# Kernel tuning notes

Measured on AMD Instinct MI355X. Metric: run time of the kernel, lower is better.

Reference implementation:

```python
import jax, jax.numpy as jnp
import numpy as np

N_NODES = 100000
N_EDGES = 1600000
D = 128


def setup_inputs() -> dict:
    key = jax.random.key(0)
    k1, k2, k3 = jax.random.split(key, 3)
    x = jax.random.normal(k1, (N_NODES, D), dtype=jnp.float32)
    edge_index = jax.random.randint(k2, (2, N_EDGES), 0, N_NODES, dtype=jnp.int64)
    weight = jax.random.normal(k3, (D, D), dtype=jnp.float32) * (1.0 / np.sqrt(D))
    bias = jnp.zeros((D,), dtype=jnp.float32)
    return {"x": x, "edge_index": edge_index, "weight": weight, "bias": bias}


def reference(x, edge_index, weight, bias):
    # Eval-mode forward: dropout(p=0.5, training=False) is identity.
    N = x.shape[0]
    row, col = edge_index[0], edge_index[1]  # source -> target

    # gcn_norm: add self loops (weight 1), symmetric normalization
    loop = jnp.arange(N, dtype=edge_index.dtype)
    full_row = jnp.concatenate([row, loop])
    full_col = jnp.concatenate([col, loop])
    ew = jnp.ones(full_row.shape[0], dtype=x.dtype)
    deg = jax.ops.segment_sum(ew, full_col, num_segments=N)
    deg_inv_sqrt = jnp.where(deg > 0, jax.lax.rsqrt(jnp.maximum(deg, 1e-12)), 0.0)
    norm = deg_inv_sqrt[full_row] * ew * deg_inv_sqrt[full_col]  # [E+N]

    # linear transform then gather-scale-scatter aggregation
    h = x @ weight.T  # [N, D]
    msgs = h[full_row] * norm[:, None]  # [E+N, D]
    out = jax.ops.segment_sum(msgs, full_col, num_segments=N)
    out = out + bias
    return jax.nn.relu(out)
```

## Files before the change

### kernel.cpp

```cpp
#include <hip/hip_runtime.h>

#define N_NODES 100000
#define N_EDGES 1600000
#define D 128
#define N_STRIPS (N_NODES / 32)

#define BSH   9
#define NBKT  196
#define P_BLK 160
#define EPB   (N_EDGES / P_BLK)

typedef __bf16 bf16x4 __attribute__((ext_vector_type(4)));
typedef __bf16 bf16x8 __attribute__((ext_vector_type(8)));
typedef float  f32x4  __attribute__((ext_vector_type(4)));

__global__ __launch_bounds__(1024) void k_prep(const int* __restrict__ col,
                                               const float4* __restrict__ w4,
                                               int* __restrict__ bhist,
                                               bf16x4* __restrict__ wb4) {
    int tid = threadIdx.x, b = blockIdx.x;
    if (b == P_BLK) {
        for (int i = tid; i < (D * D) / 4; i += 1024) {
            float4 u = w4[i];
            bf16x4 p;
            p[0] = (__bf16)u.x; p[1] = (__bf16)u.y;
            p[2] = (__bf16)u.z; p[3] = (__bf16)u.w;
            wb4[i] = p;
        }
        return;
    }
    __shared__ int lh[NBKT];
    if (tid < NBKT) lh[tid] = 0;
    __syncthreads();
    int e0 = b * EPB;
    for (int e = e0 + tid; e < e0 + EPB; e += 1024)
        atomicAdd(&lh[col[e] >> BSH], 1);
    __syncthreads();
    if (tid < NBKT) bhist[tid * P_BLK + b] = lh[tid];
}

__global__ __launch_bounds__(256) void k_bscan(int* __restrict__ bhist,
                                               int* __restrict__ gtot) {
    __shared__ int buf[256];
    int k = blockIdx.x, t = threadIdx.x;
    int v = (t < P_BLK) ? bhist[k * P_BLK + t] : 0;
    buf[t] = v;
    __syncthreads();
    for (int off = 1; off < 256; off <<= 1) {
        int u = (t >= off) ? buf[t - off] : 0;
        __syncthreads();
        buf[t] += u;
        __syncthreads();
    }
    if (t < P_BLK) bhist[k * P_BLK + t] = buf[t] - v;
    if (t == 255) gtot[k] = buf[255];
}

__global__ __launch_bounds__(256) void k_gscan(const int* __restrict__ gtot,
                                               int* __restrict__ gstart) {
    __shared__ int buf[256];
    int t = threadIdx.x;
    int v = (t < NBKT) ? gtot[t] : 0;
    buf[t] = v;
    __syncthreads();
    for (int off = 1; off < 256; off <<= 1) {
        int u = (t >= off) ? buf[t - off] : 0;
        __syncthreads();
        buf[t] += u;
        __syncthreads();
    }
    if (t < NBKT) gstart[t] = buf[t] - v;
}

__global__ __launch_bounds__(1024) void k_cscatter(const int* __restrict__ row,
                                                   const int* __restrict__ col,
                                                   const int* __restrict__ bhist,
                                                   const int* __restrict__ gstart,
                                                   unsigned* __restrict__ grec) {
    __shared__ int cur[NBKT];
    int b = blockIdx.x, t = threadIdx.x;
    if (t < NBKT) cur[t] = gstart[t] + bhist[t * P_BLK + b];
    __syncthreads();
    int e0 = b * EPB;
    for (int e = e0 + t; e < e0 + EPB; e += 1024) {
        int c = col[e];
        unsigned rec = ((unsigned)row[e] << BSH) | (unsigned)(c & ((1 << BSH) - 1));
        int pos = atomicAdd(&cur[c >> BSH], 1);
        grec[pos] = rec;
    }
}

__global__ __launch_bounds__(1024) void k_fine(const unsigned* __restrict__ grec,
                                               const int* __restrict__ gtot,
                                               const int* __restrict__ gstart,
                                               int* __restrict__ deg,
                                               float* __restrict__ dis,
                                               int* __restrict__ start,
                                               int* __restrict__ srcs) {
    __shared__ int fh[512];
    __shared__ int fscan[512];
    int b = blockIdx.x;
    int tid = threadIdx.x;
    int cnt = gtot[b];
    int gs = gstart[b];
    if (tid < 512) fh[tid] = 0;
    __syncthreads();
    for (int i = tid; i < cnt; i += 1024)
        atomicAdd(&fh[grec[gs + i] & 511], 1);
    __syncthreads();
    int v = 0;
    if (tid < 512) { v = fh[tid]; fscan[tid] = v; }
    __syncthreads();
    for (int off = 1; off < 512; off <<= 1) {
        int u = 0;
        if (tid < 512 && tid >= off) u = fscan[tid - off];
        __syncthreads();
        if (tid < 512) fscan[tid] += u;
        __syncthreads();
    }
    if (tid < 512) {
        int excl = fscan[tid] - v;
        int node = (b << BSH) + tid;
        if (node < N_NODES) {
            deg[node] = v;
            dis[node] = rsqrtf((float)v + 1.0f);
            start[node] = gs + excl;
        }
        fh[tid] = excl;
    }
    __syncthreads();
    for (int i = tid; i < cnt; i += 1024) {
        unsigned r = grec[gs + i];
        int pos = atomicAdd(&fh[r & 511], 1);
        srcs[gs + pos] = (int)(r >> BSH);
    }
}

__global__ __launch_bounds__(256) void k_hx(const float* __restrict__ x,
                                            const __bf16* __restrict__ wb,
                                            const float* __restrict__ dis,
                                            __bf16* __restrict__ hb) {
    int wave = threadIdx.x >> 6;
    int lane = threadIdx.x & 63;
    int strip = blockIdx.x * 4 + wave;
    if (strip >= N_STRIPS) return;
    int m0 = strip * 32;
    int l15 = lane & 15;
    int kq  = lane >> 4;

    bf16x8 a[2][4];
    #pragma unroll
    for (int mt = 0; mt < 2; ++mt) {
        const float* ap = x + (size_t)(m0 + mt * 16 + l15) * D + kq * 8;
        #pragma unroll
        for (int ks = 0; ks < 4; ++ks) {
            float4 lo = *(const float4*)(ap + ks * 32);
            float4 hi = *(const float4*)(ap + ks * 32 + 4);
            bf16x8 t;
            t[0] = (__bf16)lo.x; t[1] = (__bf16)lo.y;
            t[2] = (__bf16)lo.z; t[3] = (__bf16)lo.w;
            t[4] = (__bf16)hi.x; t[5] = (__bf16)hi.y;
            t[6] = (__bf16)hi.z; t[7] = (__bf16)hi.w;
            a[mt][ks] = t;
        }
    }

    f32x4 acc[2][8] = {};
    #pragma unroll
    for (int ks = 0; ks < 4; ++ks) {
        #pragma unroll
        for (int nt = 0; nt < 8; ++nt) {
            bf16x8 b = *(const bf16x8*)(wb + (size_t)(nt * 16 + l15) * D + ks * 32 + kq * 8);
            acc[0][nt] = __builtin_amdgcn_mfma_f32_16x16x32_bf16(a[0][ks], b, acc[0][nt], 0, 0, 0);
            acc[1][nt] = __builtin_amdgcn_mfma_f32_16x16x32_bf16(a[1][ks], b, acc[1][nt], 0, 0, 0);
        }
    }

    float dsv[2][4];
    #pragma unroll
    for (int mt = 0; mt < 2; ++mt)
        #pragma unroll
        for (int r = 0; r < 4; ++r)
            dsv[mt][r] = dis[m0 + mt * 16 + kq * 4 + r];

    #pragma unroll
    for (int nt = 0; nt < 8; ++nt) {
        int colj = nt * 16 + l15;
        #pragma unroll
        for (int mt = 0; mt < 2; ++mt) {
            #pragma unroll
            for (int r = 0; r < 4; ++r) {
                int rowi = m0 + mt * 16 + kq * 4 + r;
                hb[(size_t)rowi * D + colj] = (__bf16)(acc[mt][nt][r] * dsv[mt][r]);
            }
        }
    }
}

__global__ __launch_bounds__(256) void k_aggregate(const int* __restrict__ srcs,
                                                   const int* __restrict__ start,
                                                   const int* __restrict__ deg,
                                                   const __bf16* __restrict__ hb,
                                                   const float* __restrict__ dis,
                                                   const float* __restrict__ bias,
                                                   float* __restrict__ out) {
    int node = (blockIdx.x * 256 + threadIdx.x) >> 6;
    int lane = threadIdx.x & 63;
    if (node >= N_NODES) return;
    int li   = lane & 31;
    int half = lane >> 5;
    int s = start[node];
    int n = deg[node];
    float dc = dis[node];
    const unsigned char* hbase = (const unsigned char*)hb;
    size_t boff = (size_t)li * 8;

    float acc0 = 0.f, acc1 = 0.f, acc2 = 0.f, acc3 = 0.f;

    for (int base = 0; base < n; base += 64) {
        int m = n - base; if (m > 64) m = 64;
        int src_l = (lane < m) ? srcs[s + base + lane] : 0;
        int i = 0;
        for (; i + 16 <= m; i += 16) {
            int sv[8]; uint2 av[8];
            #pragma unroll
            for (int j = 0; j < 8; ++j)
                sv[j] = __shfl(src_l, i + 2 * j + half);
            #pragma unroll
            for (int j = 0; j < 8; ++j)
                av[j] = *(const uint2*)(hbase + ((size_t)sv[j] * 256 + boff));
            #pragma unroll
            for (int j = 0; j < 8; ++j) {
                acc0 += __uint_as_float(av[j].x << 16);
                acc1 += __uint_as_float(av[j].x & 0xFFFF0000u);
                acc2 += __uint_as_float(av[j].y << 16);
                acc3 += __uint_as_float(av[j].y & 0xFFFF0000u);
            }
        }
        for (; i + 2 <= m; i += 2) {
            int sj = __shfl(src_l, i + half);
            uint2 a = *(const uint2*)(hbase + ((size_t)sj * 256 + boff));
            acc0 += __uint_as_float(a.x << 16);
            acc1 += __uint_as_float(a.x & 0xFFFF0000u);
            acc2 += __uint_as_float(a.y << 16);
            acc3 += __uint_as_float(a.y & 0xFFFF0000u);
        }
        if (i < m) {
            int sj = __shfl(src_l, i);
            if (half == 0) {
                uint2 a = *(const uint2*)(hbase + ((size_t)sj * 256 + boff));
                acc0 += __uint_as_float(a.x << 16);
                acc1 += __uint_as_float(a.x & 0xFFFF0000u);
                acc2 += __uint_as_float(a.y << 16);
                acc3 += __uint_as_float(a.y & 0xFFFF0000u);
            }
        }
    }

    acc0 += __shfl_xor(acc0, 32);
    acc1 += __shfl_xor(acc1, 32);
    acc2 += __shfl_xor(acc2, 32);
    acc3 += __shfl_xor(acc3, 32);

    if (half == 0) {
        uint2 a = *(const uint2*)(hbase + ((size_t)node * 256 + boff));
        acc0 += __uint_as_float(a.x << 16);
        acc1 += __uint_as_float(a.x & 0xFFFF0000u);
        acc2 += __uint_as_float(a.y << 16);
        acc3 += __uint_as_float(a.y & 0xFFFF0000u);

        float4 b4 = *(const float4*)(bias + li * 4);
        float4 r;
        r.x = fmaxf(acc0 * dc + b4.x, 0.f);
        r.y = fmaxf(acc1 * dc + b4.y, 0.f);
        r.z = fmaxf(acc2 * dc + b4.z, 0.f);
        r.w = fmaxf(acc3 * dc + b4.w, 0.f);
        *(float4*)(out + (size_t)node * D + li * 4) = r;
    }
}

extern "C" void kernel_launch(void* const* d_in, const int* in_sizes, int n_in,
                              void* d_out, int out_size, void* d_ws, size_t ws_size,
                              hipStream_t stream) {
    const float* x    = (const float*)d_in[0];
    const int*   ei   = (const int*)d_in[1];
    const float* w    = (const float*)d_in[2];
    const float* bias = (const float*)d_in[3];
    float* out = (float*)d_out;

    char* ws = (char*)d_ws;
    int*      deg    = (int*)ws;              ws += N_NODES * 4;
    float*    dis    = (float*)ws;            ws += N_NODES * 4;
    int*      start  = (int*)ws;              ws += N_NODES * 4;
    int*      bhist  = (int*)ws;              ws += NBKT * P_BLK * 4;
    int*      gtot   = (int*)ws;              ws += 256 * 4;
    int*      gstart = (int*)ws;              ws += 256 * 4;
    __bf16*   wb     = (__bf16*)ws;           ws += D * D * 2;
    unsigned* grec   = (unsigned*)ws;         ws += (size_t)N_EDGES * 4;
    int*      srcs   = (int*)ws;              ws += (size_t)N_EDGES * 4;
    __bf16*   hb     = (__bf16*)ws;

    const int* row = ei;
    const int* col = ei + N_EDGES;

    k_prep     <<<P_BLK + 1, 1024, 0, stream>>>(col, (const float4*)w, bhist, (bf16x4*)wb);
    k_bscan    <<<NBKT, 256, 0, stream>>>(bhist, gtot);
    k_gscan    <<<1, 256, 0, stream>>>(gtot, gstart);
    k_cscatter <<<P_BLK, 1024, 0, stream>>>(row, col, bhist, gstart, grec);
    k_fine     <<<NBKT, 1024, 0, stream>>>(grec, gtot, gstart, deg, dis, start, srcs);
    k_hx       <<<(N_STRIPS + 3) / 4, 256, 0, stream>>>(x, wb, dis, hb);
    k_aggregate<<<(N_NODES * 64 + 255) / 256, 256, 0, stream>>>(srcs, start, deg, hb, dis, bias, out);
}
```

Measured before the change: 227.8 us.

## Replace two-level bucket sort CSR build with global atomic counting sort

```diff
diff --git a/kernel.cpp b/kernel.cpp
--- a/kernel.cpp
+++ b/kernel.cpp
@@ -5,22 +5,21 @@
 #define D 128
 #define N_STRIPS (N_NODES / 32)
 
-#define BSH   9
-#define NBKT  196
-#define P_BLK 160
-#define EPB   (N_EDGES / P_BLK)
+#define E4      (N_EDGES / 4)
+#define HB_BLK  391
+#define NSCB    98
 
 typedef __bf16 bf16x4 __attribute__((ext_vector_type(4)));
 typedef __bf16 bf16x8 __attribute__((ext_vector_type(8)));
 typedef float  f32x4  __attribute__((ext_vector_type(4)));
 
-__global__ __launch_bounds__(1024) void k_prep(const int* __restrict__ col,
+__global__ __launch_bounds__(1024) void k_hist(const int4* __restrict__ col4,
                                                const float4* __restrict__ w4,
-                                               int* __restrict__ bhist,
+                                               int* __restrict__ deg,
                                                bf16x4* __restrict__ wb4) {
-    int tid = threadIdx.x, b = blockIdx.x;
-    if (b == P_BLK) {
-        for (int i = tid; i < (D * D) / 4; i += 1024) {
+    int b = blockIdx.x, t = threadIdx.x;
+    if (b == HB_BLK) {
+        for (int i = t; i < (D * D) / 4; i += 1024) {
             float4 u = w4[i];
             bf16x4 p;
             p[0] = (__bf16)u.x; p[1] = (__bf16)u.y;
@@ -29,111 +28,74 @@
         }
         return;
     }
-    __shared__ int lh[NBKT];
-    if (tid < NBKT) lh[tid] = 0;
-    __syncthreads();
-    int e0 = b * EPB;
-    for (int e = e0 + tid; e < e0 + EPB; e += 1024)
-        atomicAdd(&lh[col[e] >> BSH], 1);
-    __syncthreads();
-    if (tid < NBKT) bhist[tid * P_BLK + b] = lh[tid];
-}
-
-__global__ __launch_bounds__(256) void k_bscan(int* __restrict__ bhist,
-                                               int* __restrict__ gtot) {
-    __shared__ int buf[256];
-    int k = blockIdx.x, t = threadIdx.x;
-    int v = (t < P_BLK) ? bhist[k * P_BLK + t] : 0;
+    int i = b * 1024 + t;
+    if (i < E4) {
+        int4 c = col4[i];
+        atomicAdd(&deg[c.x], 1);
+        atomicAdd(&deg[c.y], 1);
+        atomicAdd(&deg[c.z], 1);
+        atomicAdd(&deg[c.w], 1);
+    }
+}
+
+__global__ __launch_bounds__(1024) void k_scanl(const int* __restrict__ deg,
+                                                int* __restrict__ start,
+                                                int* __restrict__ btot) {
+    __shared__ int buf[1024];
+    int b = blockIdx.x, t = threadIdx.x;
+    int i = b * 1024 + t;
+    int v = (i < N_NODES) ? deg[i] : 0;
     buf[t] = v;
     __syncthreads();
-    for (int off = 1; off < 256; off <<= 1) {
+    for (int off = 1; off < 1024; off <<= 1) {
         int u = (t >= off) ? buf[t - off] : 0;
         __syncthreads();
         buf[t] += u;
         __syncthreads();
     }
-    if (t < P_BLK) bhist[k * P_BLK + t] = buf[t] - v;
-    if (t == 255) gtot[k] = buf[255];
-}
-
-__global__ __launch_bounds__(256) void k_gscan(const int* __restrict__ gtot,
-                                               int* __restrict__ gstart) {
-    __shared__ int buf[256];
-    int t = threadIdx.x;
-    int v = (t < NBKT) ? gtot[t] : 0;
-    buf[t] = v;
+    if (i < N_NODES) start[i] = buf[t] - v;
+    if (t == 1023) btot[b] = buf[1023];
+}
+
+__global__ __launch_bounds__(1024) void k_fixup(const int* __restrict__ deg,
+                                                const int* __restrict__ btot,
+                                                int* __restrict__ start,
+                                                int* __restrict__ cur,
+                                                float* __restrict__ dis) {
+    __shared__ int red[128];
+    int b = blockIdx.x, t = threadIdx.x;
+    if (t < 128) red[t] = (t < b) ? btot[t] : 0;
     __syncthreads();
-    for (int off = 1; off < 256; off <<= 1) {
-        int u = (t >= off) ? buf[t - off] : 0;
+    for (int off = 64; off > 0; off >>= 1) {
+        if (t < off) red[t] += red[t + off];
         __syncthreads();
-        buf[t] += u;
-        __syncthreads();
-    }
-    if (t < NBKT) gstart[t] = buf[t] - v;
-}
-
-__global__ __launch_bounds__(1024) void k_cscatter(const int* __restrict__ row,
-                                                   const int* __restrict__ col,
-                                                   const int* __restrict__ bhist,
-                                                   const int* __restrict__ gstart,
-                                                   unsigned* __restrict__ grec) {
-    __shared__ int cur[NBKT];
-    int b = blockIdx.x, t = threadIdx.x;
-    if (t < NBKT) cur[t] = gstart[t] + bhist[t * P_BLK + b];
-    __syncthreads();
-    int e0 = b * EPB;
-    for (int e = e0 + t; e < e0 + EPB; e += 1024) {
-        int c = col[e];
-        unsigned rec = ((unsigned)row[e] << BSH) | (unsigned)(c & ((1 << BSH) - 1));
-        int pos = atomicAdd(&cur[c >> BSH], 1);
-        grec[pos] = rec;
-    }
-}
-
-__global__ __launch_bounds__(1024) void k_fine(const unsigned* __restrict__ grec,
-                                               const int* __restrict__ gtot,
-                                               const int* __restrict__ gstart,
-                                               int* __restrict__ deg,
-                                               float* __restrict__ dis,
-                                               int* __restrict__ start,
-                                               int* __restrict__ srcs) {
-    __shared__ int fh[512];
-    __shared__ int fscan[512];
-    int b = blockIdx.x;
-    int tid = threadIdx.x;
-    int cnt = gtot[b];
-    int gs = gstart[b];
-    if (tid < 512) fh[tid] = 0;
-    __syncthreads();
-    for (int i = tid; i < cnt; i += 1024)
-        atomicAdd(&fh[grec[gs + i] & 511], 1);
-    __syncthreads();
-    int v = 0;
-    if (tid < 512) { v = fh[tid]; fscan[tid] = v; }
-    __syncthreads();
-    for (int off = 1; off < 512; off <<= 1) {
-        int u = 0;
-        if (tid < 512 && tid >= off) u = fscan[tid - off];
-        __syncthreads();
-        if (tid < 512) fscan[tid] += u;
-        __syncthreads();
-    }
-    if (tid < 512) {
-        int excl = fscan[tid] - v;
-        int node = (b << BSH) + tid;
-        if (node < N_NODES) {
-            deg[node] = v;
-            dis[node] = rsqrtf((float)v + 1.0f);
-            start[node] = gs + excl;
-        }
-        fh[tid] = excl;
-    }
-    __syncthreads();
-    for (int i = tid; i < cnt; i += 1024) {
-        unsigned r = grec[gs + i];
-        int pos = atomicAdd(&fh[r & 511], 1);
-        srcs[gs + pos] = (int)(r >> BSH);
-    }
+    }
+    int boff = red[0];
+    int i = b * 1024 + t;
+    if (i < N_NODES) {
+        int s = start[i] + boff;
+        start[i] = s;
+        cur[i]   = s;
+        dis[i]   = rsqrtf((float)deg[i] + 1.0f);
+    }
+}
+
+__global__ __launch_bounds__(1024) void k_scatter(const int4* __restrict__ row4,
+                                                  const int4* __restrict__ col4,
+                                                  int* __restrict__ cur,
+                                                  int* __restrict__ srcs) {
+    int i = blockIdx.x * 1024 + threadIdx.x;
+    if (i >= E4) return;
+    int4 r = row4[i];
+    int4 c = col4[i];
+    int p0 = atomicAdd(&cur[c.x], 1);
+    int p1 = atomicAdd(&cur[c.y], 1);
+    int p2 = atomicAdd(&cur[c.z], 1);
+    int p3 = atomicAdd(&cur[c.w], 1);
+    srcs[p0] = r.x << 8;
+    srcs[p1] = r.y << 8;
+    srcs[p2] = r.z << 8;
+    srcs[p3] = r.w << 8;
 }
 
 __global__ __launch_bounds__(256) void k_hx(const float* __restrict__ x,
@@ -228,7 +190,7 @@
                 sv[j] = __shfl(src_l, i + 2 * j + half);
             #pragma unroll
             for (int j = 0; j < 8; ++j)
-                av[j] = *(const uint2*)(hbase + ((size_t)sv[j] * 256 + boff));
+                av[j] = *(const uint2*)(hbase + ((size_t)sv[j] + boff));
             #pragma unroll
             for (int j = 0; j < 8; ++j) {
                 acc0 += __uint_as_float(av[j].x << 16);
@@ -239,7 +201,7 @@
         }
         for (; i + 2 <= m; i += 2) {
             int sj = __shfl(src_l, i + half);
-            uint2 a = *(const uint2*)(hbase + ((size_t)sj * 256 + boff));
+            uint2 a = *(const uint2*)(hbase + ((size_t)sj + boff));
             acc0 += __uint_as_float(a.x << 16);
             acc1 += __uint_as_float(a.x & 0xFFFF0000u);
             acc2 += __uint_as_float(a.y << 16);
@@ -248,7 +210,7 @@
         if (i < m) {
             int sj = __shfl(src_l, i);
             if (half == 0) {
-                uint2 a = *(const uint2*)(hbase + ((size_t)sj * 256 + boff));
+                uint2 a = *(const uint2*)(hbase + ((size_t)sj + boff));
                 acc0 += __uint_as_float(a.x << 16);
                 acc1 += __uint_as_float(a.x & 0xFFFF0000u);
                 acc2 += __uint_as_float(a.y << 16);
@@ -292,22 +254,20 @@
     int*      deg    = (int*)ws;              ws += N_NODES * 4;
     float*    dis    = (float*)ws;            ws += N_NODES * 4;
     int*      start  = (int*)ws;              ws += N_NODES * 4;
-    int*      bhist  = (int*)ws;              ws += NBKT * P_BLK * 4;
-    int*      gtot   = (int*)ws;              ws += 256 * 4;
-    int*      gstart = (int*)ws;              ws += 256 * 4;
+    int*      cur    = (int*)ws;              ws += N_NODES * 4;
+    int*      btot   = (int*)ws;              ws += 256 * 4;
     __bf16*   wb     = (__bf16*)ws;           ws += D * D * 2;
-    unsigned* grec   = (unsigned*)ws;         ws += (size_t)N_EDGES * 4;
     int*      srcs   = (int*)ws;              ws += (size_t)N_EDGES * 4;
     __bf16*   hb     = (__bf16*)ws;
 
     const int* row = ei;
     const int* col = ei + N_EDGES;
 
-    k_prep     <<<P_BLK + 1, 1024, 0, stream>>>(col, (const float4*)w, bhist, (bf16x4*)wb);
-    k_bscan    <<<NBKT, 256, 0, stream>>>(bhist, gtot);
-    k_gscan    <<<1, 256, 0, stream>>>(gtot, gstart);
-    k_cscatter <<<P_BLK, 1024, 0, stream>>>(row, col, bhist, gstart, grec);
-    k_fine     <<<NBKT, 1024, 0, stream>>>(grec, gtot, gstart, deg, dis, start, srcs);
-    k_hx       <<<(N_STRIPS + 3) / 4, 256, 0, stream>>>(x, wb, dis, hb);
+    hipMemsetAsync(deg, 0, N_NODES * 4, stream);
+    k_hist   <<<HB_BLK + 1, 1024, 0, stream>>>((const int4*)col, (const float4*)w, deg, (bf16x4*)wb);
+    k_scanl  <<<NSCB, 1024, 0, stream>>>(deg, start, btot);
+    k_fixup  <<<NSCB, 1024, 0, stream>>>(deg, btot, start, cur, dis);
+    k_scatter<<<HB_BLK, 1024, 0, stream>>>((const int4*)row, (const int4*)col, cur, srcs);
+    k_hx     <<<(N_STRIPS + 3) / 4, 256, 0, stream>>>(x, wb, dis, hb);
     k_aggregate<<<(N_NODES * 64 + 255) / 256, 256, 0, stream>>>(srcs, start, deg, hb, dis, bias, out);
 }
```

After: 369.3 us. +62.1%, slower.

## Fuse CSR-build kernels into one cooperative kernel with grid syncs and LDS edge caching

Applied to the files above, without the earlier changes.

```diff
diff --git a/kernel.cpp b/kernel.cpp
--- a/kernel.cpp
+++ b/kernel.cpp
@@ -1,4 +1,7 @@
 #include <hip/hip_runtime.h>
+#include <hip/hip_cooperative_groups.h>
+
+namespace cg = cooperative_groups;
 
 #define N_NODES 100000
 #define N_EDGES 1600000
@@ -7,19 +10,58 @@
 
 #define BSH   9
 #define NBKT  196
-#define P_BLK 160
-#define EPB   (N_EDGES / P_BLK)
+#define GRID_P 256
+#define EPB2  (N_EDGES / GRID_P)
 
 typedef __bf16 bf16x4 __attribute__((ext_vector_type(4)));
 typedef __bf16 bf16x8 __attribute__((ext_vector_type(8)));
 typedef float  f32x4  __attribute__((ext_vector_type(4)));
 
-__global__ __launch_bounds__(1024) void k_prep(const int* __restrict__ col,
+__global__ __launch_bounds__(1024) void k_part(const int* __restrict__ row,
+                                               const int* __restrict__ col,
                                                const float4* __restrict__ w4,
                                                int* __restrict__ bhist,
+                                               int* __restrict__ gtot,
+                                               int* __restrict__ gstart,
+                                               unsigned* __restrict__ grec,
+                                               int* __restrict__ srcs,
+                                               int* __restrict__ deg,
+                                               float* __restrict__ dis,
+                                               int* __restrict__ start,
                                                bf16x4* __restrict__ wb4) {
-    int tid = threadIdx.x, b = blockIdx.x;
-    if (b == P_BLK) {
+    cg::grid_group grid = cg::this_grid();
+    __shared__ int smem[13312];
+    int b = blockIdx.x, tid = threadIdx.x;
+    int* rowc = smem;
+    int* colc = smem + 6250;
+    int* aux  = smem + 12500;
+
+    if (tid < 256) aux[tid] = 0;
+    __syncthreads();
+    int e0 = b * EPB2;
+    for (int i = tid; i < EPB2; i += 1024) {
+        int r = row[e0 + i], c = col[e0 + i];
+        rowc[i] = r; colc[i] = c;
+        atomicAdd(&aux[c >> BSH], 1);
+    }
+    __syncthreads();
+    if (tid < NBKT) bhist[tid * GRID_P + b] = aux[tid];
+    grid.sync();
+
+    if (b < NBKT) {
+        int v = 0;
+        if (tid < 256) { v = bhist[b * GRID_P + tid]; aux[tid] = v; }
+        __syncthreads();
+        for (int off = 1; off < 256; off <<= 1) {
+            int u = 0;
+            if (tid < 256 && tid >= off) u = aux[tid - off];
+            __syncthreads();
+            if (tid < 256) aux[tid] += u;
+            __syncthreads();
+        }
+        if (tid < 256) bhist[b * GRID_P + tid] = aux[tid] - v;
+        if (tid == 255) gtot[b] = aux[255];
+    } else if (b == NBKT) {
         for (int i = tid; i < (D * D) / 4; i += 1024) {
             float4 u = w4[i];
             bf16x4 p;
@@ -27,112 +69,72 @@
             p[2] = (__bf16)u.z; p[3] = (__bf16)u.w;
             wb4[i] = p;
         }
-        return;
-    }
-    __shared__ int lh[NBKT];
-    if (tid < NBKT) lh[tid] = 0;
+    }
+    grid.sync();
+
+    if (b == 0) {
+        int v = 0;
+        if (tid < 256) { v = (tid < NBKT) ? gtot[tid] : 0; aux[tid] = v; }
+        __syncthreads();
+        for (int off = 1; off < 256; off <<= 1) {
+            int u = 0;
+            if (tid < 256 && tid >= off) u = aux[tid - off];
+            __syncthreads();
+            if (tid < 256) aux[tid] += u;
+            __syncthreads();
+        }
+        if (tid < NBKT) gstart[tid] = aux[tid] - v;
+    }
+    grid.sync();
+
+    if (tid < NBKT) aux[tid] = gstart[tid] + bhist[tid * GRID_P + b];
     __syncthreads();
-    int e0 = b * EPB;
-    for (int e = e0 + tid; e < e0 + EPB; e += 1024)
-        atomicAdd(&lh[col[e] >> BSH], 1);
-    __syncthreads();
-    if (tid < NBKT) bhist[tid * P_BLK + b] = lh[tid];
-}
-
-__global__ __launch_bounds__(256) void k_bscan(int* __restrict__ bhist,
-                                               int* __restrict__ gtot) {
-    __shared__ int buf[256];
-    int k = blockIdx.x, t = threadIdx.x;
-    int v = (t < P_BLK) ? bhist[k * P_BLK + t] : 0;
-    buf[t] = v;
-    __syncthreads();
-    for (int off = 1; off < 256; off <<= 1) {
-        int u = (t >= off) ? buf[t - off] : 0;
-        __syncthreads();
-        buf[t] += u;
-        __syncthreads();
-    }
-    if (t < P_BLK) bhist[k * P_BLK + t] = buf[t] - v;
-    if (t == 255) gtot[k] = buf[255];
-}
-
-__global__ __launch_bounds__(256) void k_gscan(const int* __restrict__ gtot,
-                                               int* __restrict__ gstart) {
-    __shared__ int buf[256];
-    int t = threadIdx.x;
-    int v = (t < NBKT) ? gtot[t] : 0;
-    buf[t] = v;
-    __syncthreads();
-    for (int off = 1; off < 256; off <<= 1) {
-        int u = (t >= off) ? buf[t - off] : 0;
-        __syncthreads();
-        buf[t] += u;
-        __syncthreads();
-    }
-    if (t < NBKT) gstart[t] = buf[t] - v;
-}
-
-__global__ __launch_bounds__(1024) void k_cscatter(const int* __restrict__ row,
-                                                   const int* __restrict__ col,
-                                                   const int* __restrict__ bhist,
-                                                   const int* __restrict__ gstart,
-                                                   unsigned* __restrict__ grec) {
-    __shared__ int cur[NBKT];
-    int b = blockIdx.x, t = threadIdx.x;
-    if (t < NBKT) cur[t] = gstart[t] + bhist[t * P_BLK + b];
-    __syncthreads();
-    int e0 = b * EPB;
-    for (int e = e0 + t; e < e0 + EPB; e += 1024) {
-        int c = col[e];
-        unsigned rec = ((unsigned)row[e] << BSH) | (unsigned)(c & ((1 << BSH) - 1));
-        int pos = atomicAdd(&cur[c >> BSH], 1);
-        grec[pos] = rec;
-    }
-}
-
-__global__ __launch_bounds__(1024) void k_fine(const unsigned* __restrict__ grec,
-                                               const int* __restrict__ gtot,
-                                               const int* __restrict__ gstart,
-                                               int* __restrict__ deg,
-                                               float* __restrict__ dis,
-                                               int* __restrict__ start,
-                                               int* __restrict__ srcs) {
-    __shared__ int fh[512];
-    __shared__ int fscan[512];
-    int b = blockIdx.x;
-    int tid = threadIdx.x;
-    int cnt = gtot[b];
-    int gs = gstart[b];
-    if (tid < 512) fh[tid] = 0;
-    __syncthreads();
-    for (int i = tid; i < cnt; i += 1024)
-        atomicAdd(&fh[grec[gs + i] & 511], 1);
-    __syncthreads();
-    int v = 0;
-    if (tid < 512) { v = fh[tid]; fscan[tid] = v; }
-    __syncthreads();
-    for (int off = 1; off < 512; off <<= 1) {
-        int u = 0;
-        if (tid < 512 && tid >= off) u = fscan[tid - off];
-        __syncthreads();
-        if (tid < 512) fscan[tid] += u;
-        __syncthreads();
-    }
-    if (tid < 512) {
-        int excl = fscan[tid] - v;
-        int node = (b << BSH) + tid;
-        if (node < N_NODES) {
-            deg[node] = v;
-            dis[node] = rsqrtf((float)v + 1.0f);
-            start[node] = gs + excl;
-        }
-        fh[tid] = excl;
-    }
-    __syncthreads();
-    for (int i = tid; i < cnt; i += 1024) {
-        unsigned r = grec[gs + i];
-        int pos = atomicAdd(&fh[r & 511], 1);
-        srcs[gs + pos] = (int)(r >> BSH);
+    for (int i = tid; i < EPB2; i += 1024) {
+        int c = colc[i];
+        int pos = atomicAdd(&aux[c >> BSH], 1);
+        grec[pos] = ((unsigned)rowc[i] << BSH) | (unsigned)(c & ((1 << BSH) - 1));
+    }
+    grid.sync();
+
+    if (b < NBKT) {
+        int cnt = gtot[b], gs = gstart[b];
+        int* cache = smem;
+        int* fh    = smem + 12288;
+        int* fsc   = smem + 12800;
+        if (tid < 512) fh[tid] = 0;
+        __syncthreads();
+        for (int i = tid; i < cnt; i += 1024) {
+            unsigned r = grec[gs + i];
+            if (i < 12288) cache[i] = (int)r;
+            atomicAdd(&fh[r & 511], 1);
+        }
+        __syncthreads();
+        int v = 0;
+        if (tid < 512) { v = fh[tid]; fsc[tid] = v; }
+        __syncthreads();
+        for (int off = 1; off < 512; off <<= 1) {
+            int u = 0;
+            if (tid < 512 && tid >= off) u = fsc[tid - off];
+            __syncthreads();
+            if (tid < 512) fsc[tid] += u;
+            __syncthreads();
+        }
+        if (tid < 512) {
+            int excl = fsc[tid] - v;
+            int node = (b << BSH) + tid;
+            if (node < N_NODES) {
+                deg[node]   = v;
+                dis[node]   = rsqrtf((float)v + 1.0f);
+                start[node] = gs + excl;
+            }
+            fh[tid] = excl;
+        }
+        __syncthreads();
+        for (int i = tid; i < cnt; i += 1024) {
+            unsigned r = (i < 12288) ? (unsigned)cache[i] : grec[gs + i];
+            int pos = atomicAdd(&fh[r & 511], 1);
+            srcs[gs + pos] = (int)((r >> BSH) << 8);
+        }
     }
 }
 
@@ -228,7 +230,7 @@
                 sv[j] = __shfl(src_l, i + 2 * j + half);
             #pragma unroll
             for (int j = 0; j < 8; ++j)
-                av[j] = *(const uint2*)(hbase + ((size_t)sv[j] * 256 + boff));
+                av[j] = *(const uint2*)(hbase + ((size_t)sv[j] + boff));
             #pragma unroll
             for (int j = 0; j < 8; ++j) {
                 acc0 += __uint_as_float(av[j].x << 16);
@@ -239,7 +241,7 @@
         }
         for (; i + 2 <= m; i += 2) {
             int sj = __shfl(src_l, i + half);
-            uint2 a = *(const uint2*)(hbase + ((size_t)sj * 256 + boff));
+            uint2 a = *(const uint2*)(hbase + ((size_t)sj + boff));
             acc0 += __uint_as_float(a.x << 16);
             acc1 += __uint_as_float(a.x & 0xFFFF0000u);
             acc2 += __uint_as_float(a.y << 16);
@@ -248,7 +250,7 @@
         if (i < m) {
             int sj = __shfl(src_l, i);
             if (half == 0) {
-                uint2 a = *(const uint2*)(hbase + ((size_t)sj * 256 + boff));
+                uint2 a = *(const uint2*)(hbase + ((size_t)sj + boff));
                 acc0 += __uint_as_float(a.x << 16);
                 acc1 += __uint_as_float(a.x & 0xFFFF0000u);
                 acc2 += __uint_as_float(a.y << 16);
@@ -292,7 +294,7 @@
     int*      deg    = (int*)ws;              ws += N_NODES * 4;
     float*    dis    = (float*)ws;            ws += N_NODES * 4;
     int*      start  = (int*)ws;              ws += N_NODES * 4;
-    int*      bhist  = (int*)ws;              ws += NBKT * P_BLK * 4;
+    int*      bhist  = (int*)ws;              ws += NBKT * GRID_P * 4;
     int*      gtot   = (int*)ws;              ws += 256 * 4;
     int*      gstart = (int*)ws;              ws += 256 * 4;
     __bf16*   wb     = (__bf16*)ws;           ws += D * D * 2;
@@ -302,12 +304,14 @@
 
     const int* row = ei;
     const int* col = ei + N_EDGES;
-
-    k_prep     <<<P_BLK + 1, 1024, 0, stream>>>(col, (const float4*)w, bhist, (bf16x4*)wb);
-    k_bscan    <<<NBKT, 256, 0, stream>>>(bhist, gtot);
-    k_gscan    <<<1, 256, 0, stream>>>(gtot, gstart);
-    k_cscatter <<<P_BLK, 1024, 0, stream>>>(row, col, bhist, gstart, grec);
-    k_fine     <<<NBKT, 1024, 0, stream>>>(grec, gtot, gstart, deg, dis, start, srcs);
+    const float4* w4 = (const float4*)w;
+    bf16x4* wb4 = (bf16x4*)wb;
+
+    void* kargs[] = {(void*)&row, (void*)&col, (void*)&w4, (void*)&bhist,
+                     (void*)&gtot, (void*)&gstart, (void*)&grec, (void*)&srcs,
+                     (void*)&deg, (void*)&dis, (void*)&start, (void*)&wb4};
+    hipLaunchCooperativeKernel((const void*)k_part, dim3(GRID_P), dim3(1024),
+                               kargs, 0, stream);
     k_hx       <<<(N_STRIPS + 3) / 4, 256, 0, stream>>>(x, wb, dis, hb);
     k_aggregate<<<(N_NODES * 64 + 255) / 256, 256, 0, stream>>>(srcs, start, deg, hb, dis, bias, out);
 }
```

Result: slower. 349.4 us (+53.4%).

## Fuse fine CSR scatter into aggregation via per-block shared-memory source lists

Applied to the files above, without the earlier changes.

```diff
diff --git a/kernel.cpp b/kernel.cpp
--- a/kernel.cpp
+++ b/kernel.cpp
@@ -9,6 +9,7 @@
 #define NBKT  196
 #define P_BLK 160
 #define EPB   (N_EDGES / P_BLK)
+#define SL_CAP 6144
 
 typedef __bf16 bf16x4 __attribute__((ext_vector_type(4)));
 typedef __bf16 bf16x8 __attribute__((ext_vector_type(8)));
@@ -90,15 +91,14 @@
     }
 }
 
-__global__ __launch_bounds__(1024) void k_fine(const unsigned* __restrict__ grec,
-                                               const int* __restrict__ gtot,
-                                               const int* __restrict__ gstart,
-                                               int* __restrict__ deg,
-                                               float* __restrict__ dis,
-                                               int* __restrict__ start,
-                                               int* __restrict__ srcs) {
+__global__ __launch_bounds__(1024) void k_fine2(const unsigned* __restrict__ grec,
+                                                const int* __restrict__ gtot,
+                                                const int* __restrict__ gstart,
+                                                int* __restrict__ deg,
+                                                float* __restrict__ dis,
+                                                int* __restrict__ start) {
     __shared__ int fh[512];
-    __shared__ int fscan[512];
+    __shared__ int fsc[512];
     int b = blockIdx.x;
     int tid = threadIdx.x;
     int cnt = gtot[b];
@@ -109,30 +109,22 @@
         atomicAdd(&fh[grec[gs + i] & 511], 1);
     __syncthreads();
     int v = 0;
-    if (tid < 512) { v = fh[tid]; fscan[tid] = v; }
+    if (tid < 512) { v = fh[tid]; fsc[tid] = v; }
     __syncthreads();
     for (int off = 1; off < 512; off <<= 1) {
         int u = 0;
-        if (tid < 512 && tid >= off) u = fscan[tid - off];
-        __syncthreads();
-        if (tid < 512) fscan[tid] += u;
+        if (tid < 512 && tid >= off) u = fsc[tid - off];
+        __syncthreads();
+        if (tid < 512) fsc[tid] += u;
         __syncthreads();
     }
     if (tid < 512) {
-        int excl = fscan[tid] - v;
         int node = (b << BSH) + tid;
         if (node < N_NODES) {
-            deg[node] = v;
-            dis[node] = rsqrtf((float)v + 1.0f);
-            start[node] = gs + excl;
-        }
-        fh[tid] = excl;
-    }
-    __syncthreads();
-    for (int i = tid; i < cnt; i += 1024) {
-        unsigned r = grec[gs + i];
-        int pos = atomicAdd(&fh[r & 511], 1);
-        srcs[gs + pos] = (int)(r >> BSH);
+            deg[node]   = v;
+            dis[node]   = rsqrtf((float)v + 1.0f);
+            start[node] = gs + fsc[tid] - v;
+        }
     }
 }
 
@@ -197,85 +189,124 @@
     }
 }
 
-__global__ __launch_bounds__(256) void k_aggregate(const int* __restrict__ srcs,
+__global__ __launch_bounds__(512) void k_aggregate(const unsigned* __restrict__ grec,
+                                                   const int* __restrict__ gtot,
+                                                   const int* __restrict__ gstart,
                                                    const int* __restrict__ start,
                                                    const int* __restrict__ deg,
                                                    const __bf16* __restrict__ hb,
                                                    const float* __restrict__ dis,
                                                    const float* __restrict__ bias,
                                                    float* __restrict__ out) {
-    int node = (blockIdx.x * 256 + threadIdx.x) >> 6;
-    int lane = threadIdx.x & 63;
-    if (node >= N_NODES) return;
+    __shared__ int srcsL[SL_CAP];
+    __shared__ int cur[128];
+    __shared__ int sbase_s;
+    int blk = blockIdx.x;
+    int b  = blk >> 2;
+    int sl = blk & 3;
+    int cnt = gtot[b];
+    int gs  = gstart[b];
+    int node0 = (b << BSH) + sl * 128;
+    int t = threadIdx.x;
+
+    if (t == 0)
+        sbase_s = (node0 < N_NODES) ? start[node0] : gs + cnt;
+    if (t < 128) {
+        int nd = node0 + t;
+        cur[t] = (nd < N_NODES) ? start[nd] : gs + cnt;
+    }
+    __syncthreads();
+    int sbase = sbase_s;
+    if (t < 128) cur[t] -= sbase;
+    __syncthreads();
+
+    int lo = sl * 128;
+    for (int i = t; i < cnt; i += 512) {
+        unsigned r = grec[gs + i];
+        int s = (int)(r & 511) - lo;
+        if ((unsigned)s < 128u) {
+            int p = atomicAdd(&cur[s], 1);
+            if (p < SL_CAP) srcsL[p] = (int)((r >> BSH) << 8);
+        }
+    }
+    __syncthreads();
+
+    int wave = t >> 6;
+    int lane = t & 63;
     int li   = lane & 31;
     int half = lane >> 5;
-    int s = start[node];
-    int n = deg[node];
-    float dc = dis[node];
     const unsigned char* hbase = (const unsigned char*)hb;
     size_t boff = (size_t)li * 8;
 
-    float acc0 = 0.f, acc1 = 0.f, acc2 = 0.f, acc3 = 0.f;
-
-    for (int base = 0; base < n; base += 64) {
-        int m = n - base; if (m > 64) m = 64;
-        int src_l = (lane < m) ? srcs[s + base + lane] : 0;
-        int i = 0;
-        for (; i + 16 <= m; i += 16) {
-            int sv[8]; uint2 av[8];
-            #pragma unroll
-            for (int j = 0; j < 8; ++j)
-                sv[j] = __shfl(src_l, i + 2 * j + half);
-            #pragma unroll
-            for (int j = 0; j < 8; ++j)
-                av[j] = *(const uint2*)(hbase + ((size_t)sv[j] * 256 + boff));
-            #pragma unroll
-            for (int j = 0; j < 8; ++j) {
-                acc0 += __uint_as_float(av[j].x << 16);
-                acc1 += __uint_as_float(av[j].x & 0xFFFF0000u);
-                acc2 += __uint_as_float(av[j].y << 16);
-                acc3 += __uint_as_float(av[j].y & 0xFFFF0000u);
+    for (int k = 0; k < 16; ++k) {
+        int nd = node0 + wave * 16 + k;
+        if (nd >= N_NODES) break;
+        int n  = deg[nd];
+        int s0 = start[nd] - sbase;
+        float dc = dis[nd];
+
+        float acc0 = 0.f, acc1 = 0.f, acc2 = 0.f, acc3 = 0.f;
+
+        for (int base = 0; base < n; base += 64) {
+            int m = n - base; if (m > 64) m = 64;
+            int src_l = (lane < m) ? srcsL[s0 + base + lane] : 0;
+            int i = 0;
+            for (; i + 16 <= m; i += 16) {
+                int sv[8]; uint2 av[8];
+                #pragma unroll
+                for (int j = 0; j < 8; ++j)
+                    sv[j] = __shfl(src_l, i + 2 * j + half);
+                #pragma unroll
+                for (int j = 0; j < 8; ++j)
+                    av[j] = *(const uint2*)(hbase + ((size_t)sv[j] + boff));
+                #pragma unroll
+                for (int j = 0; j < 8; ++j) {
+                    acc0 += __uint_as_float(av[j].x << 16);
+                    acc1 += __uint_as_float(av[j].x & 0xFFFF0000u);
+                    acc2 += __uint_as_float(av[j].y << 16);
+                    acc3 += __uint_as_float(av[j].y & 0xFFFF0000u);
+                }
             }
-        }
-        for (; i + 2 <= m; i += 2) {
-            int sj = __shfl(src_l, i + half);
-            uint2 a = *(const uint2*)(hbase + ((size_t)sj * 256 + boff));
-            acc0 += __uint_as_float(a.x << 16);
-            acc1 += __uint_as_float(a.x & 0xFFFF0000u);
-            acc2 += __uint_as_float(a.y << 16);
-            acc3 += __uint_as_float(a.y & 0xFFFF0000u);
-        }
-        if (i < m) {
-            int sj = __shfl(src_l, i);
-            if (half == 0) {
-                uint2 a = *(const uint2*)(hbase + ((size_t)sj * 256 + boff));
+            for (; i + 2 <= m; i += 2) {
+                int sj = __shfl(src_l, i + half);
+                uint2 a = *(const uint2*)(hbase + ((size_t)sj + boff));
                 acc0 += __uint_as_float(a.x << 16);
                 acc1 += __uint_as_float(a.x & 0xFFFF0000u);
                 acc2 += __uint_as_float(a.y << 16);
                 acc3 += __uint_as_float(a.y & 0xFFFF0000u);
             }
-        }
-    }
-
-    acc0 += __shfl_xor(acc0, 32);
-    acc1 += __shfl_xor(acc1, 32);
-    acc2 += __shfl_xor(acc2, 32);
-    acc3 += __shfl_xor(acc3, 32);
-
-    if (half == 0) {
-        uint2 a = *(const uint2*)(hbase + ((size_t)node * 256 + boff));
-        acc0 += __uint_as_float(a.x << 16);
-        acc1 += __uint_as_float(a.x & 0xFFFF0000u);
-        acc2 += __uint_as_float(a.y << 16);
-        acc3 += __uint_as_float(a.y & 0xFFFF0000u);
-
-        float4 b4 = *(const float4*)(bias + li * 4);
-        float4 r;
-        r.x = fmaxf(acc0 * dc + b4.x, 0.f);
-        r.y = fmaxf(acc1 * dc + b4.y, 0.f);
-        r.z = fmaxf(acc2 * dc + b4.z, 0.f);
-        r.w = fmaxf(acc3 * dc + b4.w, 0.f);
-        *(float4*)(out + (size_t)node * D + li * 4) = r;
+            if (i < m) {
+                int sj = __shfl(src_l, i);
+                if (half == 0) {
+                    uint2 a = *(const uint2*)(hbase + ((size_t)sj + boff));
+                    acc0 += __uint_as_float(a.x << 16);
+                    acc1 += __uint_as_float(a.x & 0xFFFF0000u);
+                    acc2 += __uint_as_float(a.y << 16);
+                    acc3 += __uint_as_float(a.y & 0xFFFF0000u);
+                }
+            }
+        }
+
+        acc0 += __shfl_xor(acc0, 32);
+        acc1 += __shfl_xor(acc1, 32);
+        acc2 += __shfl_xor(acc2, 32);
+        acc3 += __shfl_xor(acc3, 32);
+
+        if (half == 0) {
+            uint2 a = *(const uint2*)(hbase + ((size_t)nd * 256 + boff));
+            acc0 += __uint_as_float(a.x << 16);
+            acc1 += __uint_as_float(a.x & 0xFFFF0000u);
+            acc2 += __uint_as_float(a.y << 16);
+            acc3 += __uint_as_float(a.y & 0xFFFF0000u);
+
+            float4 b4 = *(const float4*)(bias + li * 4);
+            float4 r;
+            r.x = fmaxf(acc0 * dc + b4.x, 0.f);
+            r.y = fmaxf(acc1 * dc + b4.y, 0.f);
+            r.z = fmaxf(acc2 * dc + b4.z, 0.f);
+            r.w = fmaxf(acc3 * dc + b4.w, 0.f);
+            *(float4*)(out + (size_t)nd * D + li * 4) = r;
+        }
     }
 }
 
@@ -297,7 +328,6 @@
     int*      gstart = (int*)ws;              ws += 256 * 4;
     __bf16*   wb     = (__bf16*)ws;           ws += D * D * 2;
     unsigned* grec   = (unsigned*)ws;         ws += (size_t)N_EDGES * 4;
-    int*      srcs   = (int*)ws;              ws += (size_t)N_EDGES * 4;
     __bf16*   hb     = (__bf16*)ws;
 
     const int* row = ei;
@@ -307,7 +337,7 @@
     k_bscan    <<<NBKT, 256, 0, stream>>>(bhist, gtot);
     k_gscan    <<<1, 256, 0, stream>>>(gtot, gstart);
     k_cscatter <<<P_BLK, 1024, 0, stream>>>(row, col, bhist, gstart, grec);
-    k_fine     <<<NBKT, 1024, 0, stream>>>(grec, gtot, gstart, deg, dis, start, srcs);
+    k_fine2    <<<NBKT, 1024, 0, stream>>>(grec, gtot, gstart, deg, dis, start);
     k_hx       <<<(N_STRIPS + 3) / 4, 256, 0, stream>>>(x, wb, dis, hb);
-    k_aggregate<<<(N_NODES * 64 + 255) / 256, 256, 0, stream>>>(srcs, start, deg, hb, dis, bias, out);
-}
+    k_aggregate<<<NBKT * 4, 512, 0, stream>>>(grec, gtot, gstart, start, deg, hb, dis, bias, out);
+}
```

After: 234.6 us. +3.0%, slower.
